# Optimization experiments

Hardware: AMD Instinct MI355X
Metric: run time of the kernel (lower is better)

Reference implementation:

```python
import jax, jax.numpy as jnp
import numpy as np

B, S, D = 1, 2048, 2048
HQ, HKV = 32, 8
HD = D // HQ            # 64
G = HQ // HKV           # 4 query heads per kv head


def setup_inputs() -> dict:
    key = jax.random.key(0)
    ks = jax.random.split(key, 5)
    x = jax.random.normal(ks[0], (B, S, D), jnp.float32)
    # RoPE tables (theta = 10000), shape [S, HD//2]
    inv_freq = 1.0 / (10000.0 ** (np.arange(0, HD, 2, dtype=np.float64) / HD))
    angles = np.outer(np.arange(S, dtype=np.float64), inv_freq)
    freqs_cos = jnp.asarray(np.cos(angles), jnp.float32)
    freqs_sin = jnp.asarray(np.sin(angles), jnp.float32)
    # additive causal mask [1,1,S,S]: 0 on/below diagonal, large negative above
    i = jnp.arange(S)
    causal_mask = jnp.where(i[None, :] <= i[:, None], 0.0, -1e9).astype(jnp.float32)[None, None]
    sc = 1.0 / np.sqrt(D)
    Wq = jax.random.normal(ks[1], (D, HQ * HD), jnp.float32) * sc
    Wk = jax.random.normal(ks[2], (D, HKV * HD), jnp.float32) * sc
    Wv = jax.random.normal(ks[3], (D, HKV * HD), jnp.float32) * sc
    Wo = jax.random.normal(ks[4], (D, D), jnp.float32) * sc
    return {"x": x, "freqs_cos": freqs_cos, "freqs_sin": freqs_sin,
            "causal_mask": causal_mask, "Wq": Wq, "Wk": Wk, "Wv": Wv, "Wo": Wo}


def _rope(t, cos, sin):
    # t: [B,S,H,HD]; complex multiply on interleaved (even, odd) pairs
    b, s, h, d = t.shape
    t2 = t.reshape(b, s, h, d // 2, 2)
    t0, t1 = t2[..., 0], t2[..., 1]
    c = cos[None, :, None, :]
    sn = sin[None, :, None, :]
    out = jnp.stack([t0 * c - t1 * sn, t0 * sn + t1 * c], axis=-1)
    return out.reshape(b, s, h, d)


def reference(x, freqs_cos, freqs_sin, causal_mask, Wq, Wk, Wv, Wo):
    b, s, _ = x.shape
    q = (x @ Wq).reshape(b, s, HQ, HD)
    k = (x @ Wk).reshape(b, s, HKV, HD)
    v = (x @ Wv).reshape(b, s, HKV, HD)
    q = _rope(q, freqs_cos, freqs_sin)
    k = _rope(k, freqs_cos, freqs_sin)
    # GQA without materializing repeat_kv: group query heads per kv head
    q = q.transpose(0, 2, 1, 3).reshape(b, HKV, G, s, HD)   # [b,kv,g,s,d]
    k = k.transpose(0, 2, 1, 3)                              # [b,kv,s,d]
    v = v.transpose(0, 2, 1, 3)                              # [b,kv,s,d]
    scores = jnp.einsum('bkgsd,bktd->bkgst', q, k) / jnp.sqrt(jnp.float32(HD))
    scores = scores + causal_mask[:, :, None]                # [1,1,1,S,S] broadcast
    probs = jax.nn.softmax(scores, axis=-1)
    out = jnp.einsum('bkgst,bktd->bkgsd', probs, v)          # [b,kv,g,s,d]
    out = out.transpose(0, 3, 1, 2, 4).reshape(b, s, D)      # merge heads in (kv,g) order
    return out @ Wo
```

## Files before the change

kernel.cpp:

```cpp
#include <hip/hip_runtime.h>

#define SEQ 2048
#define DMODEL 2048

typedef __attribute__((ext_vector_type(8))) _Float16 half8;
typedef __attribute__((ext_vector_type(4))) float f32x4;
typedef __attribute__((ext_vector_type(16))) float f32x16;

typedef const __attribute__((address_space(1))) void* gptr_t;
typedef __attribute__((address_space(3))) void* lptr_t;

static __device__ __forceinline__ void gload16(const void* g, void* l) {
  __builtin_amdgcn_global_load_lds((gptr_t)g, (lptr_t)l, 16, 0, 0);
}

static __device__ __forceinline__ unsigned short f2h(float f) {
  _Float16 h = (_Float16)f;
  union { _Float16 h; unsigned short u; } v; v.h = h;
  return v.u;
}

static __device__ __forceinline__ unsigned int pkh2(float a, float b) {
  union { __fp16 __attribute__((ext_vector_type(2))) h; unsigned int u; } v;
  v.h = __builtin_amdgcn_cvt_pkrtz(a, b);
  return v.u;
}

__global__ void k_cvt(const float* __restrict__ in, unsigned short* __restrict__ out, int n) {
  int i = (blockIdx.x * 256 + threadIdx.x) * 4;
  if (i >= n) return;
  float4 v = *(const float4*)(in + i);
  ushort4 o;
  o.x = f2h(v.x); o.y = f2h(v.y); o.z = f2h(v.z); o.w = f2h(v.w);
  *(ushort4*)(out + i) = o;
}

__global__ void k_tcvt(const float* __restrict__ in, unsigned short* __restrict__ out,
                       int K, int N, int ldin) {
  __shared__ float tile[32][33];
  int n0 = blockIdx.x * 32, k0 = blockIdx.y * 32;
  int tx = threadIdx.x, ty = threadIdx.y;
  #pragma unroll
  for (int j = ty; j < 32; j += 8)
    tile[j][tx] = in[(long)(k0 + j) * ldin + n0 + tx];
  __syncthreads();
  #pragma unroll
  for (int j = ty; j < 32; j += 8)
    out[(long)(n0 + j) * K + k0 + tx] = f2h(tile[tx][j]);
}

__global__ void k_tvp(const unsigned short* __restrict__ in, unsigned short* __restrict__ out) {
  __shared__ unsigned short tile[32][33];
  int c0 = blockIdx.x * 32, s0 = blockIdx.y * 32;
  int tx = threadIdx.x, ty = threadIdx.y;
  #pragma unroll
  for (int j = ty; j < 32; j += 8)
    tile[j][tx] = in[(long)(s0 + j) * 512 + c0 + tx];
  __syncthreads();
  #pragma unroll
  for (int j = ty; j < 32; j += 8) {
    int c = c0 + j;
    int s = s0 + tx;
    int sp = (s & ~12) | ((s & 8) >> 1) | ((s & 4) << 1);
    out[((long)(c >> 6) * 64 + (c & 63)) * SEQ + sp] = tile[tx][j];
  }
}

static __device__ __forceinline__ bool gemm_core(const unsigned short* __restrict__ A,
                                                 const unsigned short* __restrict__ B,
                                                 int K, char* SM, long m0, long n0,
                                                 int& wmO, int& wnO, f32x4 acc[4][4]) {
  int t = threadIdx.x;
  int l = t & 63, w = t >> 6;
  int ks = w & 1, wm = (w >> 2) & 1, wn = (w >> 1) & 1;
  int lr = l & 15, lh = l >> 4;
  wmO = wm; wnO = wn;
  unsigned short* As = (unsigned short*)SM;
  unsigned short* Bs = (unsigned short*)(SM + 32768);

  const unsigned short* Ag = A + (m0 + (t >> 3)) * K + (((t & 7) ^ ((t >> 3) & 7)) * 8);
  const unsigned short* Bg = B + (n0 + (t >> 3)) * K + (((t & 7) ^ ((t >> 3) & 7)) * 8);

  #pragma unroll
  for (int i = 0; i < 4; i++)
    #pragma unroll
    for (int j = 0; j < 4; j++)
      acc[i][j] = (f32x4){0.f, 0.f, 0.f, 0.f};

#define STG(buf, k0) do { \
    gload16(Ag + (k0), As + (buf) * 8192 + t * 8); \
    gload16(Ag + 64 * K + (k0), As + (buf) * 8192 + 4096 + t * 8); \
    gload16(Bg + (k0), Bs + (buf) * 8192 + t * 8); \
    gload16(Bg + 64 * K + (k0), Bs + (buf) * 8192 + 4096 + t * 8); \
  } while (0)

  int T = K >> 6;
  STG(0, 0);
  asm volatile("s_waitcnt vmcnt(0)" ::: "memory");
  __builtin_amdgcn_s_barrier();

  for (int ph = 0; ph < T; ph++) {
    if (ph + 1 < T) STG((ph + 1) & 1, (ph + 1) * 64);
    const unsigned short* Ab = As + (ph & 1) * 8192;
    const unsigned short* Bb = Bs + (ph & 1) * 8192;
    half8 a[4], b[4];
    #pragma unroll
    for (int mf = 0; mf < 4; mf++) {
      int ra = wm * 64 + mf * 16 + lr;
      a[mf] = *(const half8*)&Ab[ra * 64 + (((ks * 4 + lh) ^ (ra & 7)) * 8)];
    }
    #pragma unroll
    for (int nf = 0; nf < 4; nf++) {
      int rb = wn * 64 + nf * 16 + lr;
      b[nf] = *(const half8*)&Bb[rb * 64 + (((ks * 4 + lh) ^ (rb & 7)) * 8)];
    }
    #pragma unroll
    for (int mf = 0; mf < 4; mf++)
      #pragma unroll
      for (int nf = 0; nf < 4; nf++)
        acc[mf][nf] = __builtin_amdgcn_mfma_f32_16x16x32_f16(a[mf], b[nf], acc[mf][nf], 0, 0, 0);
    asm volatile("s_waitcnt vmcnt(0)" ::: "memory");
    __builtin_amdgcn_s_barrier();
  }
#undef STG

  __syncthreads();
  float* red = (float*)SM;
  int p = wm * 2 + wn;
  if (ks == 1) {
    #pragma unroll
    for (int mf = 0; mf < 4; mf++)
      #pragma unroll
      for (int nf = 0; nf < 4; nf++)
        *(f32x4*)&red[p * 4096 + l * 64 + (((mf * 4 + nf) ^ (l & 15)) << 2)] = acc[mf][nf];
  }
  __syncthreads();
  if (ks == 0) {
    #pragma unroll
    for (int mf = 0; mf < 4; mf++)
      #pragma unroll
      for (int nf = 0; nf < 4; nf++)
        acc[mf][nf] += *(const f32x4*)&red[p * 4096 + l * 64 + (((mf * 4 + nf) ^ (l & 15)) << 2)];
  }
  return ks == 0;
}

__global__ __launch_bounds__(512) void k_gemm(const unsigned short* __restrict__ A,
                                              const unsigned short* __restrict__ B,
                                              float* __restrict__ C, int M, int N, int K) {
  __shared__ __align__(16) char SM[65536];
  int l = threadIdx.x & 63;
  int lr = l & 15, lh = l >> 4;
  long m0 = (long)blockIdx.y * 128, n0 = (long)blockIdx.x * 128;
  f32x4 acc[4][4];
  int wm, wn;
  bool own = gemm_core(A, B, K, SM, m0, n0, wm, wn, acc);
  if (own) {
    #pragma unroll
    for (int mf = 0; mf < 4; mf++)
      #pragma unroll
      for (int nf = 0; nf < 4; nf++)
        #pragma unroll
        for (int i = 0; i < 4; i++)
          C[(m0 + wm * 64 + mf * 16 + lh * 4 + i) * N + n0 + wn * 64 + nf * 16 + lr] = acc[mf][nf][i];
  }
}

__global__ __launch_bounds__(512) void k_gemm_qkv(const unsigned short* __restrict__ A,
                                                  const unsigned short* __restrict__ B,
                                                  unsigned short* __restrict__ Qr,
                                                  unsigned short* __restrict__ Kr,
                                                  unsigned short* __restrict__ Vr,
                                                  const float* __restrict__ fc,
                                                  const float* __restrict__ fs, int K) {
  __shared__ __align__(16) char SM[65536];
  int l = threadIdx.x & 63;
  int lr = l & 15, lh = l >> 4;
  long m0 = (long)blockIdx.y * 128, n0 = (long)blockIdx.x * 128;
  f32x4 acc[4][4];
  int wm, wn;
  bool own = gemm_core(A, B, K, SM, m0, n0, wm, wn, acc);
  if (!own) return;

  const float SC = 0.125f * 1.44269504f;
  int n0i = (int)n0;
  if (n0i < 2560) {
    bool isQ = n0i < 2048;
    float scl = isQ ? SC : 1.0f;
    #pragma unroll
    for (int mf = 0; mf < 4; mf++)
      #pragma unroll
      for (int i = 0; i < 4; i++) {
        int row = (int)m0 + wm * 64 + mf * 16 + lh * 4 + i;
        const float* fcr = fc + row * 32;
        const float* fsr = fs + row * 32;
        #pragma unroll
        for (int nf = 0; nf < 4; nf++) {
          float v = acc[mf][nf][i];
          float pv = __shfl_xor(v, 1);
          int col = n0i + wn * 64 + nf * 16 + lr;
          int j = (col & 63) >> 1;
          float c_ = fcr[j] * scl, s_ = fsr[j] * scl;
          float o = (lr & 1) ? (pv * s_ + v * c_) : (v * c_ - pv * s_);
          if (isQ) Qr[(long)row * 2048 + col] = f2h(o);
          else {
            int cc = col - 2048;
            Kr[((long)(cc >> 6) * SEQ + row) * 64 + (cc & 63)] = f2h(o);
          }
        }
      }
  } else {
    #pragma unroll
    for (int mf = 0; mf < 4; mf++)
      #pragma unroll
      for (int i = 0; i < 4; i++) {
        int row = (int)m0 + wm * 64 + mf * 16 + lh * 4 + i;
        #pragma unroll
        for (int nf = 0; nf < 4; nf++) {
          int col = n0i + wn * 64 + nf * 16 + lr;
          Vr[(long)row * 512 + (col - 2560)] = f2h(acc[mf][nf][i]);
        }
      }
  }
}

template <bool DG>
static __device__ __forceinline__ void attn_tile(const unsigned short* __restrict__ Ks,
                                                 const unsigned short* __restrict__ Vs,
                                                 int q, int hs, const half8 (&Qf)[4],
                                                 f32x16& O0, f32x16& O1, f32x4& lsum4) {
  half8 Kf[4], Vf[2][2];
  #pragma unroll
  for (int d = 0; d < 4; d++) {
    int e0 = d * 16 + 8 * hs;
    Kf[d] = *(const half8*)&Ks[q * 64 + (e0 ^ ((q & 7) << 3))];
  }
  #pragma unroll
  for (int ks = 0; ks < 2; ks++)
    #pragma unroll
    for (int nf = 0; nf < 2; nf++)
      Vf[ks][nf] = *(const half8*)&Vs[(2 * ks + hs) * 512 + (q + 32 * nf) * 8];

  f32x16 S;
  #pragma unroll
  for (int r = 0; r < 16; r++) S[r] = 0.f;
  #pragma unroll
  for (int d = 0; d < 4; d++)
    S = __builtin_amdgcn_mfma_f32_32x32x16_f16(Kf[d], Qf[d], S, 0, 0, 0);

  float p[16];
  #pragma unroll
  for (int r = 0; r < 16; r++) {
    float v = S[r];
    if (DG) {
      int key = (r & 3) + 8 * (r >> 2) + 4 * hs;
      if (key > q) v = -1e30f;
    }
    p[r] = __builtin_exp2f(v - 8.0f);
    lsum4[r & 3] += p[r];
  }

  union { unsigned int u[4]; half8 hh; } f0, f1;
  #pragma unroll
  for (int c = 0; c < 4; c++) {
    f0.u[c] = pkh2(p[2 * c], p[2 * c + 1]);
    f1.u[c] = pkh2(p[8 + 2 * c], p[9 + 2 * c]);
  }

  O0 = __builtin_amdgcn_mfma_f32_32x32x16_f16(f0.hh, Vf[0][0], O0, 0, 0, 0);
  O0 = __builtin_amdgcn_mfma_f32_32x32x16_f16(f1.hh, Vf[1][0], O0, 0, 0, 0);
  O1 = __builtin_amdgcn_mfma_f32_32x32x16_f16(f0.hh, Vf[0][1], O1, 0, 0, 0);
  O1 = __builtin_amdgcn_mfma_f32_32x32x16_f16(f1.hh, Vf[1][1], O1, 0, 0, 0);
}

__global__ __launch_bounds__(256) void k_attn(const unsigned short* __restrict__ Qr,
                                              const unsigned short* __restrict__ Kr,
                                              const unsigned short* __restrict__ Vg,
                                              unsigned short* __restrict__ Op,
                                              float* __restrict__ Lp) {
  __shared__ unsigned short KT[2][8192];
  __shared__ unsigned short VT[2][8192];

  int tt = threadIdx.x;
  int wid = tt >> 6, l = tt & 63;
  int q = l & 31, hs = l >> 5;
  int h = blockIdx.x, hkv = h >> 2;
  int y = blockIdx.y;
  int by = 15 - (y >> 1), z = y & 1;
  int h8 = (by + 2) >> 1;
  int sb = z ? h8 : 0, se = z ? by + 1 : h8;
  int dt = 4 * by + wid;
  int q0 = by * 128 + wid * 32;

  const unsigned short* Kh = Kr + (long)hkv * SEQ * 64;
  const unsigned short* Vh = Vg + (long)hkv * 64 * SEQ;

  int skr = tt >> 3, skc = tt & 7;
  const unsigned short* Ksrc = Kh + (long)skr * 64 + ((skc * 8) ^ ((skr & 7) << 3));
  const unsigned short* Vsrc = Vh + (long)(tt & 63) * SEQ + ((tt >> 6) * 8);

#define ASTAGE(si) do { \
    int buf_ = (si) & 1; \
    _Pragma("unroll") for (int sub_ = 0; sub_ < 4; sub_++) { \
      int t0_ = ((si) * 4 + sub_) * 32; \
      gload16(Ksrc + (long)t0_ * 64, &KT[buf_][sub_ * 2048 + tt * 8]); \
      gload16(Vsrc + t0_, &VT[buf_][sub_ * 2048 + tt * 8]); \
    } \
  } while (0)

  half8 Qf[4];
  #pragma unroll
  for (int d = 0; d < 4; d++)
    Qf[d] = *(const half8*)&Qr[(long)(q0 + q) * 2048 + h * 64 + d * 16 + 8 * hs];

  f32x16 O0, O1;
  #pragma unroll
  for (int r = 0; r < 16; r++) { O0[r] = 0.f; O1[r] = 0.f; }
  f32x4 lsum4 = (f32x4){0.f, 0.f, 0.f, 0.f};

  if (sb < se) {
    ASTAGE(sb);
    asm volatile("s_waitcnt vmcnt(0)" ::: "memory");
    __builtin_amdgcn_s_barrier();

    for (int si = sb; si < se; si++) {
      if (si + 1 < se) ASTAGE(si + 1);

      int buf = si & 1;
      const unsigned short* Kb = &KT[buf][0];
      const unsigned short* Vb = &VT[buf][0];
      int rem = dt - si * 4 + 1;
      if (rem > 4) {
        attn_tile<false>(Kb, Vb, q, hs, Qf, O0, O1, lsum4);
        attn_tile<false>(Kb + 2048, Vb + 2048, q, hs, Qf, O0, O1, lsum4);
        attn_tile<false>(Kb + 4096, Vb + 4096, q, hs, Qf, O0, O1, lsum4);
        attn_tile<false>(Kb + 6144, Vb + 6144, q, hs, Qf, O0, O1, lsum4);
      } else if (rem > 0) {
        for (int sub = 0; sub < rem - 1; sub++)
          attn_tile<false>(Kb + sub * 2048, Vb + sub * 2048, q, hs, Qf, O0, O1, lsum4);
        attn_tile<true>(Kb + (rem - 1) * 2048, Vb + (rem - 1) * 2048, q, hs, Qf, O0, O1, lsum4);
      }

      asm volatile("s_waitcnt vmcnt(0)" ::: "memory");
      __builtin_amdgcn_s_barrier();
    }
  }
#undef ASTAGE

  float ls = lsum4[0] + lsum4[1] + lsum4[2] + lsum4[3];
  ls += __shfl_xor(ls, 32);
  if (l < 32) Lp[z * 65536 + h * 2048 + q0 + l] = ls;
  unsigned short* Oz = Op + (long)z * 2048 * 2048;
  #pragma unroll
  for (int r = 0; r < 16; r++) {
    int row = (r & 3) + 8 * (r >> 2) + 4 * hs;
    Oz[(long)(q0 + row) * 2048 + h * 64 + q] = f2h(O0[r]);
    Oz[(long)(q0 + row) * 2048 + h * 64 + q + 32] = f2h(O1[r]);
  }
}

__global__ void k_merge(const unsigned short* __restrict__ Op, const float* __restrict__ Lp,
                        unsigned short* __restrict__ AO) {
  int row = blockIdx.x, t = threadIdx.x;
  int col = t * 8, h = col >> 6;
  float li = 1.f / (Lp[h * 2048 + row] + Lp[65536 + h * 2048 + row]);
  half8 a = *(const half8*)&Op[(long)row * 2048 + col];
  half8 b = *(const half8*)&Op[4194304l + (long)row * 2048 + col];
  half8 o;
  #pragma unroll
  for (int j = 0; j < 8; j++)
    o[j] = (_Float16)(((float)a[j] + (float)b[j]) * li);
  *(half8*)&AO[(long)row * 2048 + col] = o;
}

extern "C" void kernel_launch(void* const* d_in, const int* in_sizes, int n_in,
                              void* d_out, int out_size, void* d_ws, size_t ws_size,
                              hipStream_t stream) {
  const float* x  = (const float*)d_in[0];
  const float* fc = (const float*)d_in[1];
  const float* fs = (const float*)d_in[2];
  const float* Wq = (const float*)d_in[4];
  const float* Wk = (const float*)d_in[5];
  const float* Wv = (const float*)d_in[6];
  const float* Wo = (const float*)d_in[7];
  float* out = (float*)d_out;

  char* ws = (char*)d_ws;
  unsigned short* xb  = (unsigned short*)(ws);
  unsigned short* WT  = (unsigned short*)(ws + (8l  << 20));
  unsigned short* WoT = (unsigned short*)(ws + (20l << 20));
  unsigned short* Qr  = (unsigned short*)(ws + (28l << 20));
  unsigned short* Kr  = (unsigned short*)(ws + (36l << 20));
  unsigned short* Vr  = (unsigned short*)(ws + (38l << 20));
  unsigned short* Vt  = (unsigned short*)(ws + (40l << 20));
  unsigned short* Opp = (unsigned short*)(ws + (44l << 20));
  float*          Lp  = (float*)(ws + (60l << 20));
  unsigned short* AO  = xb;

  dim3 tb(32, 8);
  k_cvt<<<4096, 256, 0, stream>>>(x, xb, 2048 * 2048);
  k_tcvt<<<dim3(64, 64), tb, 0, stream>>>(Wq, WT, 2048, 2048, 2048);
  k_tcvt<<<dim3(16, 64), tb, 0, stream>>>(Wk, WT + 2048l * 2048, 2048, 512, 512);
  k_tcvt<<<dim3(16, 64), tb, 0, stream>>>(Wv, WT + 2560l * 2048, 2048, 512, 512);
  k_tcvt<<<dim3(64, 64), tb, 0, stream>>>(Wo, WoT, 2048, 2048, 2048);

  k_gemm_qkv<<<dim3(24, 16), 512, 0, stream>>>(xb, WT, Qr, Kr, Vr, fc, fs, 2048);

  k_tvp<<<dim3(16, 64), tb, 0, stream>>>(Vr, Vt);

  k_attn<<<dim3(32, 32), 256, 0, stream>>>(Qr, Kr, Vt, Opp, Lp);
  k_merge<<<2048, 256, 0, stream>>>(Opp, Lp, AO);

  k_gemm<<<dim3(16, 16), 512, 0, stream>>>(AO, WoT, out, 2048, 2048, 2048);
}
```

Measured before the change: 151.7 us.

## Narrow QKV GEMM tiles to 128x96 and swizzle block order for L2 reuse

The QKV projection GEMM now uses 128x96 output tiles, so 512 blocks launch instead of 384, which gives more even coverage of the 256 CUs. The epilogue now decides per column whether to apply RoPE for Q/K or write V, since tile boundaries no longer line up with the 2048/2560 split. Both GEMMs also remap block indices with a stride-8 swizzle so that concurrently running blocks share A/B panels in L2. In exchange, the smaller tiles reuse each loaded operand less, and the QKV epilogue branches on every column.

Result: no change. 149.1 us (-1.7%).

```diff
diff --git a/kernel.cpp b/kernel.cpp
--- a/kernel.cpp
+++ b/kernel.cpp
@@ -66,10 +66,12 @@
   }
 }
 
+template <int NF>
 static __device__ __forceinline__ bool gemm_core(const unsigned short* __restrict__ A,
                                                  const unsigned short* __restrict__ B,
                                                  int K, char* SM, long m0, long n0,
-                                                 int& wmO, int& wnO, f32x4 acc[4][4]) {
+                                                 int& wmO, int& wnO, f32x4 acc[4][NF]) {
+  constexpr int BN = NF * 32;
   int t = threadIdx.x;
   int l = t & 63, w = t >> 6;
   int ks = w & 1, wm = (w >> 2) & 1, wn = (w >> 1) & 1;
@@ -84,14 +86,14 @@
   #pragma unroll
   for (int i = 0; i < 4; i++)
     #pragma unroll
-    for (int j = 0; j < 4; j++)
+    for (int j = 0; j < NF; j++)
       acc[i][j] = (f32x4){0.f, 0.f, 0.f, 0.f};
 
 #define STG(buf, k0) do { \
     gload16(Ag + (k0), As + (buf) * 8192 + t * 8); \
     gload16(Ag + 64 * K + (k0), As + (buf) * 8192 + 4096 + t * 8); \
-    gload16(Bg + (k0), Bs + (buf) * 8192 + t * 8); \
-    gload16(Bg + 64 * K + (k0), Bs + (buf) * 8192 + 4096 + t * 8); \
+    gload16(Bg + (k0), Bs + (buf) * (BN * 64) + t * 8); \
+    if (t < (BN - 64) * 8) gload16(Bg + 64 * K + (k0), Bs + (buf) * (BN * 64) + 4096 + t * 8); \
   } while (0)
 
   int T = K >> 6;
@@ -102,22 +104,22 @@
   for (int ph = 0; ph < T; ph++) {
     if (ph + 1 < T) STG((ph + 1) & 1, (ph + 1) * 64);
     const unsigned short* Ab = As + (ph & 1) * 8192;
-    const unsigned short* Bb = Bs + (ph & 1) * 8192;
-    half8 a[4], b[4];
+    const unsigned short* Bb = Bs + (ph & 1) * (BN * 64);
+    half8 a[4], b[NF];
     #pragma unroll
     for (int mf = 0; mf < 4; mf++) {
       int ra = wm * 64 + mf * 16 + lr;
       a[mf] = *(const half8*)&Ab[ra * 64 + (((ks * 4 + lh) ^ (ra & 7)) * 8)];
     }
     #pragma unroll
-    for (int nf = 0; nf < 4; nf++) {
-      int rb = wn * 64 + nf * 16 + lr;
+    for (int nf = 0; nf < NF; nf++) {
+      int rb = wn * (NF * 16) + nf * 16 + lr;
       b[nf] = *(const half8*)&Bb[rb * 64 + (((ks * 4 + lh) ^ (rb & 7)) * 8)];
     }
     #pragma unroll
     for (int mf = 0; mf < 4; mf++)
       #pragma unroll
-      for (int nf = 0; nf < 4; nf++)
+      for (int nf = 0; nf < NF; nf++)
         acc[mf][nf] = __builtin_amdgcn_mfma_f32_16x16x32_f16(a[mf], b[nf], acc[mf][nf], 0, 0, 0);
     asm volatile("s_waitcnt vmcnt(0)" ::: "memory");
     __builtin_amdgcn_s_barrier();
@@ -131,7 +133,7 @@
     #pragma unroll
     for (int mf = 0; mf < 4; mf++)
       #pragma unroll
-      for (int nf = 0; nf < 4; nf++)
+      for (int nf = 0; nf < NF; nf++)
         *(f32x4*)&red[p * 4096 + l * 64 + (((mf * 4 + nf) ^ (l & 15)) << 2)] = acc[mf][nf];
   }
   __syncthreads();
@@ -139,7 +141,7 @@
     #pragma unroll
     for (int mf = 0; mf < 4; mf++)
       #pragma unroll
-      for (int nf = 0; nf < 4; nf++)
+      for (int nf = 0; nf < NF; nf++)
         acc[mf][nf] += *(const f32x4*)&red[p * 4096 + l * 64 + (((mf * 4 + nf) ^ (l & 15)) << 2)];
   }
   return ks == 0;
@@ -151,10 +153,12 @@
   __shared__ __align__(16) char SM[65536];
   int l = threadIdx.x & 63;
   int lr = l & 15, lh = l >> 4;
-  long m0 = (long)blockIdx.y * 128, n0 = (long)blockIdx.x * 128;
+  int bid = blockIdx.y * 16 + blockIdx.x;
+  int swz = (bid & 7) * 32 + (bid >> 3);
+  long m0 = (long)(swz >> 4) * 128, n0 = (long)(swz & 15) * 128;
   f32x4 acc[4][4];
   int wm, wn;
-  bool own = gemm_core(A, B, K, SM, m0, n0, wm, wn, acc);
+  bool own = gemm_core<4>(A, B, K, SM, m0, n0, wm, wn, acc);
   if (own) {
     #pragma unroll
     for (int mf = 0; mf < 4; mf++)
@@ -176,52 +180,44 @@
   __shared__ __align__(16) char SM[65536];
   int l = threadIdx.x & 63;
   int lr = l & 15, lh = l >> 4;
-  long m0 = (long)blockIdx.y * 128, n0 = (long)blockIdx.x * 128;
-  f32x4 acc[4][4];
+  int bid = blockIdx.y * 32 + blockIdx.x;
+  int swz = (bid & 7) * 64 + (bid >> 3);
+  long m0 = (long)(swz >> 5) * 128, n0 = (long)(swz & 31) * 96;
+  f32x4 acc[4][3];
   int wm, wn;
-  bool own = gemm_core(A, B, K, SM, m0, n0, wm, wn, acc);
+  bool own = gemm_core<3>(A, B, K, SM, m0, n0, wm, wn, acc);
   if (!own) return;
 
   const float SC = 0.125f * 1.44269504f;
   int n0i = (int)n0;
-  if (n0i < 2560) {
-    bool isQ = n0i < 2048;
-    float scl = isQ ? SC : 1.0f;
-    #pragma unroll
-    for (int mf = 0; mf < 4; mf++)
+  #pragma unroll
+  for (int mf = 0; mf < 4; mf++)
+    #pragma unroll
+    for (int i = 0; i < 4; i++) {
+      int row = (int)m0 + wm * 64 + mf * 16 + lh * 4 + i;
+      const float* fcr = fc + row * 32;
+      const float* fsr = fs + row * 32;
       #pragma unroll
-      for (int i = 0; i < 4; i++) {
-        int row = (int)m0 + wm * 64 + mf * 16 + lh * 4 + i;
-        const float* fcr = fc + row * 32;
-        const float* fsr = fs + row * 32;
-        #pragma unroll
-        for (int nf = 0; nf < 4; nf++) {
-          float v = acc[mf][nf][i];
+      for (int nf = 0; nf < 3; nf++) {
+        float v = acc[mf][nf][i];
+        int col = n0i + wn * 48 + nf * 16 + lr;
+        if (col < 2560) {
           float pv = __shfl_xor(v, 1);
-          int col = n0i + wn * 64 + nf * 16 + lr;
+          float scl = col < 2048 ? SC : 1.0f;
           int j = (col & 63) >> 1;
           float c_ = fcr[j] * scl, s_ = fsr[j] * scl;
           float o = (lr & 1) ? (pv * s_ + v * c_) : (v * c_ - pv * s_);
-          if (isQ) Qr[(long)row * 2048 + col] = f2h(o);
-          else {
+          if (col < 2048) {
+            Qr[(long)row * 2048 + col] = f2h(o);
+          } else {
             int cc = col - 2048;
             Kr[((long)(cc >> 6) * SEQ + row) * 64 + (cc & 63)] = f2h(o);
           }
+        } else {
+          Vr[(long)row * 512 + (col - 2560)] = f2h(v);
         }
       }
-  } else {
-    #pragma unroll
-    for (int mf = 0; mf < 4; mf++)
-      #pragma unroll
-      for (int i = 0; i < 4; i++) {
-        int row = (int)m0 + wm * 64 + mf * 16 + lh * 4 + i;
-        #pragma unroll
-        for (int nf = 0; nf < 4; nf++) {
-          int col = n0i + wn * 64 + nf * 16 + lr;
-          Vr[(long)row * 512 + (col - 2560)] = f2h(acc[mf][nf][i]);
-        }
-      }
-  }
+    }
 }
 
 template <bool DG>
@@ -404,7 +400,7 @@
   k_tcvt<<<dim3(16, 64), tb, 0, stream>>>(Wv, WT + 2560l * 2048, 2048, 512, 512);
   k_tcvt<<<dim3(64, 64), tb, 0, stream>>>(Wo, WoT, 2048, 2048, 2048);
 
-  k_gemm_qkv<<<dim3(24, 16), 512, 0, stream>>>(xb, WT, Qr, Kr, Vr, fc, fs, 2048);
+  k_gemm_qkv<<<dim3(32, 16), 512, 0, stream>>>(xb, WT, Qr, Kr, Vr, fc, fs, 2048);
 
   k_tvp<<<dim3(16, 64), tb, 0, stream>>>(Vr, Vt);
 
```
